# Performance work log

Hardware: AMD Instinct MI355X
Metric: run time of the kernel (lower is better)

The kernel has to match this reference:

```python
import jax, jax.numpy as jnp
import numpy as np

# Keras GRUCell (reset_after=True, default in TF2) step
# Keras LSTMCell step (gate order i, f, c, o)
# Keras RNN masking semantics: at masked steps, states are frozen and the
# step output is the previous output (equivalent to freezing every layer's h).

def _gru_step(a, h, W, U, bi, br):
    gx = a @ W + bi          # [B, 3H] input projection
    gh = h @ U + br          # [B, 3H] recurrent projection (reset_after)
    xz, xr, xh = jnp.split(gx, 3, axis=-1)
    rz, rr, rh = jnp.split(gh, 3, axis=-1)
    z = jax.nn.sigmoid(xz + rz)
    r = jax.nn.sigmoid(xr + rr)
    hh = jnp.tanh(xh + r * rh)
    return z * h + (1.0 - z) * hh


def _lstm_step(a, h, c, W, U, b):
    g = a @ W + h @ U + b    # [B, 4H]
    gi, gf, gc, go = jnp.split(g, 4, axis=-1)
    i = jax.nn.sigmoid(gi)
    f = jax.nn.sigmoid(gf)
    cn = f * c + i * jnp.tanh(gc)
    hn = jax.nn.sigmoid(go) * jnp.tanh(cn)
    return hn, cn


def run_gru_stack(x, mask, layers):
    # x: [B,T,D], mask: [B,T] bool; layers: list of (W,U,bi,br)
    B = x.shape[0]
    H = layers[0][1].shape[0]
    xT = jnp.swapaxes(x, 0, 1)      # [T,B,D]
    mT = jnp.swapaxes(mask, 0, 1)   # [T,B]

    def step(hs, inp):
        xt, mt = inp
        a = xt
        new = []
        for (W, U, bi, br), h in zip(layers, hs):
            hn = _gru_step(a, h, W, U, bi, br)
            hn = jnp.where(mt[:, None], hn, h)  # freeze state under mask
            new.append(hn)
            a = hn
        return tuple(new), a

    h0 = tuple(jnp.zeros((B, H), x.dtype) for _ in layers)
    _, ys = jax.lax.scan(step, h0, (xT, mT))
    return jnp.swapaxes(ys, 0, 1)   # [B,T,H]


def run_lstm_stack(x, mask, layers):
    # layers: list of (W,U,b)
    B = x.shape[0]
    H = layers[0][1].shape[0]
    xT = jnp.swapaxes(x, 0, 1)
    mT = jnp.swapaxes(mask, 0, 1)

    def step(state, inp):
        xt, mt = inp
        a = xt
        new = []
        for (W, U, b), (h, c) in zip(layers, state):
            hn, cn = _lstm_step(a, h, c, W, U, b)
            hn = jnp.where(mt[:, None], hn, h)
            cn = jnp.where(mt[:, None], cn, c)
            new.append((hn, cn))
            a = hn
        return tuple(new), a

    s0 = tuple((jnp.zeros((B, H), x.dtype), jnp.zeros((B, H), x.dtype)) for _ in layers)
    _, ys = jax.lax.scan(step, s0, (xT, mT))
    return jnp.swapaxes(ys, 0, 1)


def _forward(x, lengths, g_W0, g_U0, g_bi0, g_br0, g_W1, g_U1, g_bi1, g_br1,
             l_W0, l_U0, l_b0, l_W1, l_U1, l_b1, out_W, out_b):
    T = x.shape[1]
    mask = jnp.arange(T)[None, :] < lengths[:, None]          # [B,T]
    o1 = run_gru_stack(x, mask, [(g_W0, g_U0, g_bi0, g_br0),
                                 (g_W1, g_U1, g_bi1, g_br1)])  # [B,T,H]
    o2 = run_lstm_stack(x, mask, [(l_W0, l_U0, l_b0),
                                  (l_W1, l_U1, l_b1)])          # [B,T,H]
    c = jnp.concatenate([o1, o2], axis=-1)                      # [B,T,2H]
    return c @ out_W + out_b                                    # [B,T,1]


def setup_inputs() -> dict:
    key = jax.random.key(0)
    ks = jax.random.split(key, 16)
    B, T, D, H = 64, 512, 96, 256
    glorot = lambda k, shp: (jax.random.normal(k, shp, dtype=jnp.float32)
                             / np.sqrt(shp[0]).astype(np.float32))
    inp = {
        "x": jax.random.normal(ks[0], (B, T, D), dtype=jnp.float32),
        "lengths": jax.random.randint(ks[1], (B,), 1, T + 1),
        # GRU stack (reset_after: separate input/recurrent biases)
        "g_W0": glorot(ks[2], (D, 3 * H)),
        "g_U0": glorot(ks[3], (H, 3 * H)),
        "g_bi0": jnp.zeros((3 * H,), jnp.float32),
        "g_br0": jnp.zeros((3 * H,), jnp.float32),
        "g_W1": glorot(ks[4], (H, 3 * H)),
        "g_U1": glorot(ks[5], (H, 3 * H)),
        "g_bi1": jnp.zeros((3 * H,), jnp.float32),
        "g_br1": jnp.zeros((3 * H,), jnp.float32),
        # LSTM stack
        "l_W0": glorot(ks[6], (D, 4 * H)),
        "l_U0": glorot(ks[7], (H, 4 * H)),
        "l_b0": jnp.zeros((4 * H,), jnp.float32),
        "l_W1": glorot(ks[8], (H, 4 * H)),
        "l_U1": glorot(ks[9], (H, 4 * H)),
        "l_b1": jnp.zeros((4 * H,), jnp.float32),
        # Dense head on concat [.., 2H] -> 1
        "out_W": glorot(ks[10], (2 * H, 1)),
        "out_b": jnp.zeros((1,), jnp.float32),
    }
    return inp


def reference(x, lengths, g_W0, g_U0, g_bi0, g_br0, g_W1, g_U1, g_bi1, g_br1,
              l_W0, l_U0, l_b0, l_W1, l_U1, l_b1, out_W, out_b):
    return _forward(x, lengths, g_W0, g_U0, g_bi0, g_br0, g_W1, g_U1, g_bi1,
                    g_br1, l_W0, l_U0, l_b0, l_W1, l_U1, l_b1, out_W, out_b)
```

## Files before the change

kernel.cpp:

```cpp
#include <hip/hip_runtime.h>
#include <hip/hip_fp16.h>

constexpr int Tt = 512, Dd = 96, Hh = 256;
constexpr int NS0 = 16;
constexpr int NSP = 8;
typedef unsigned long long u64;

constexpr size_t OFF_P0  = (size_t)4 << 20;
constexpr size_t OFF_P1  = (size_t)12 << 20;
constexpr size_t OFF_FLG = (size_t)20 << 20;
constexpr size_t OFF_W16 = ((size_t)20 << 20) + ((size_t)64 << 10);
constexpr size_t oGW0 = 0;
constexpr size_t oGU0 = oGW0 + (size_t)48 * 768;
constexpr size_t oGW1 = oGU0 + (size_t)128 * 768;
constexpr size_t oGU1 = oGW1 + (size_t)128 * 768;
constexpr size_t oLW0 = oGU1 + (size_t)128 * 768;
constexpr size_t oLU0 = oLW0 + (size_t)48 * 1024;
constexpr size_t oLW1 = oLU0 + (size_t)128 * 1024;
constexpr size_t oLU1 = oLW1 + (size_t)128 * 1024;

constexpr int SMEM_BYTES = 2048 + 65536 + 64;

__device__ __forceinline__ float sigf(float v) { return 1.0f / (1.0f + __expf(-v)); }
__device__ __forceinline__ u64 agld(const u64* p) {
    return __hip_atomic_load(p, __ATOMIC_RELAXED, __HIP_MEMORY_SCOPE_AGENT);
}
__device__ __forceinline__ int agldi(const int* p) {
    return __hip_atomic_load(p, __ATOMIC_ACQUIRE, __HIP_MEMORY_SCOPE_AGENT);
}
__device__ __forceinline__ void agst(u64* p, u64 v) {
    __hip_atomic_store(p, v, __ATOMIC_RELAXED, __HIP_MEMORY_SCOPE_AGENT);
}

__device__ __forceinline__ float dot2f(unsigned w, unsigned a, float acc) {
#if __has_builtin(__builtin_amdgcn_fdot2)
    typedef _Float16 h2v __attribute__((ext_vector_type(2)));
    h2v wh, ah;
    __builtin_memcpy(&wh, &w, 4);
    __builtin_memcpy(&ah, &a, 4);
    return __builtin_amdgcn_fdot2(wh, ah, acc, false);
#else
    const float2 wf = __half22float2(*(const __half2*)&w);
    const float2 af = __half22float2(*(const __half2*)&a);
    acc = fmaf(wf.x, af.x, acc);
    return fmaf(wf.y, af.y, acc);
#endif
}

__device__ __forceinline__ int hidx(int k, int r) {
    return (k >> 1) * 8 + r * 2 + (k & 1);
}

template<int G>
__device__ __forceinline__ void load4h(uint4* wv, const uint4* __restrict__ M4,
                                       int ldm, int kpb) {
    const int base = (kpb >> 2) * ldm;
    #pragma unroll
    for (int g = 0; g < G; ++g)
        wv[g] = M4[base + g * 256];
}
template<int G>
__device__ __forceinline__ void fma4h(const uint4* wv, const uint4* __restrict__ A4,
                                      int kpb, float4* acc) {
    const uint4 a0 = A4[kpb + 0];
    const uint4 a1 = A4[kpb + 1];
    const uint4 a2 = A4[kpb + 2];
    const uint4 a3 = A4[kpb + 3];
    #pragma unroll
    for (int g = 0; g < G; ++g) {
        const uint4 w = wv[g];
        acc[g].x = dot2f(w.x, a0.x, acc[g].x);
        acc[g].y = dot2f(w.x, a0.y, acc[g].y);
        acc[g].z = dot2f(w.x, a0.z, acc[g].z);
        acc[g].w = dot2f(w.x, a0.w, acc[g].w);
        acc[g].x = dot2f(w.y, a1.x, acc[g].x);
        acc[g].y = dot2f(w.y, a1.y, acc[g].y);
        acc[g].z = dot2f(w.y, a1.z, acc[g].z);
        acc[g].w = dot2f(w.y, a1.w, acc[g].w);
        acc[g].x = dot2f(w.z, a2.x, acc[g].x);
        acc[g].y = dot2f(w.z, a2.y, acc[g].y);
        acc[g].z = dot2f(w.z, a2.z, acc[g].z);
        acc[g].w = dot2f(w.z, a2.w, acc[g].w);
        acc[g].x = dot2f(w.w, a3.x, acc[g].x);
        acc[g].y = dot2f(w.w, a3.y, acc[g].y);
        acc[g].z = dot2f(w.w, a3.z, acc[g].z);
        acc[g].w = dot2f(w.w, a3.w, acc[g].w);
    }
}
template<int G>
__device__ __forceinline__ void gemmP(const uint4* __restrict__ M4, int ldm,
                                      const uint4* __restrict__ A4,
                                      int kp0, int kp1, float4* acc) {
    const int n4 = (kp1 - kp0) >> 2;
    uint4 wv0[G], wv1[G];
    if (n4 <= 0) return;
    load4h<G>(wv0, M4, ldm, kp0);
    int c2 = 0;
    for (; c2 + 2 <= n4; c2 += 2) {
        load4h<G>(wv1, M4, ldm, kp0 + (c2 + 1) * 4);
        fma4h<G>(wv0, A4, kp0 + c2 * 4, acc);
        if (c2 + 2 < n4) load4h<G>(wv0, M4, ldm, kp0 + (c2 + 2) * 4);
        fma4h<G>(wv1, A4, kp0 + (c2 + 1) * 4, acc);
    }
    if (c2 < n4) fma4h<G>(wv0, A4, kp0 + c2 * 4, acc);
}

__global__ void cvt_pair(const float* __restrict__ src, unsigned* __restrict__ dst,
                         int n, int ld) {
    const int i = blockIdx.x * 256 + threadIdx.x;
    if (i >= n) return;
    const int kp = i / ld, col = i - kp * ld;
    const __half2 h = __floats2half2_rn(src[(2 * kp) * ld + col],
                                        src[(2 * kp + 1) * ld + col]);
    dst[((size_t)((kp >> 2) * ld + col) << 2) + (kp & 3)] = *(const unsigned*)&h;
}

__global__ void __launch_bounds__(1024, 4)
rnn_persist(const float* __restrict__ x, const int* __restrict__ lengths,
            const float* __restrict__ gbi0, const float* __restrict__ gbr0,
            const float* __restrict__ gbi1, const float* __restrict__ gbr1,
            const float* __restrict__ lb0, const float* __restrict__ lb1,
            const float* __restrict__ outW, const float* __restrict__ outb,
            float* __restrict__ out, char* __restrict__ wsb)
{
    extern __shared__ __align__(16) char smem[];
    unsigned* sAh = (unsigned*)smem;
    float* sG   = (float*)(smem + 2048);
    float* sRed = (float*)(smem + 2048 + 65536);
    __half* sAhh = (__half*)sAh;
    const uint4* A4 = (const uint4*)sAh;

    const int tid = threadIdx.x;
    const int c   = tid & 255;
    const int grp = tid >> 8;
    const int bx  = blockIdx.x;
    const int role  = bx & 3;
    const int chain = (bx >> 2) & 1;
    const int rg    = bx >> 3;
    const int rowbase = rg * 4;

    const int GA  = chain ? 4 : 3;
    const int GAH = GA * Hh;

    u64* h0ring = (u64*)wsb + (size_t)(chain * 16 + rg) * (NS0 * 1024);
    u64* p0ring = (u64*)(wsb + OFF_P0) + (size_t)(chain * 16 + rg) * (NSP * 4096);
    u64* p1ring = (u64*)(wsb + OFF_P1) + (size_t)(chain * 16 + rg) * (NSP * 4096);
    int* flags = (int*)(wsb + OFF_FLG);
    int* flg_r0 = flags + ((chain * 16 + rg) * 4 + 1) * 32;
    int* flg_p1 = flags + ((chain * 16 + rg) * 4 + 2) * 32;
    int* flg_r1 = flags + ((chain * 16 + rg) * 4 + 3) * 32;

    const unsigned* W16 = (const unsigned*)(wsb + OFF_W16);
    size_t woff;
    if (chain == 0) woff = (role == 0) ? oGW0 : (role == 1) ? oGU0 : (role == 2) ? oGW1 : oGU1;
    else            woff = (role == 0) ? oLW0 : (role == 1) ? oLU0 : (role == 2) ? oLW1 : oLU1;
    const uint4* M4 = (const uint4*)(W16 + woff) + c;

    const int KR  = (role == 0) ? Dd : Hh;
    const int KP2 = KR >> 3;
    const int kp0 = grp * KP2, kp1 = kp0 + KP2;

    const int NP  = 4 * GAH;
    const int npt = NP >> 10;
    float biasv[4];
    int sgidx[4];
    if (role == 0 || role == 2) {
        const float* bsrc = (chain == 0) ? (role == 0 ? gbi0 : gbi1)
                                         : (role == 0 ? lb0 : lb1);
        #pragma unroll
        for (int i = 0; i < 4; ++i) {
            if (i < npt) {
                const int e = tid + i * 1024;
                const int r = e / GAH, rem = e - r * GAH;
                biasv[i] = bsrc[rem];
                sgidx[i] = r * 1024 + rem;
            } else { biasv[i] = 0; sgidx[i] = 0; }
        }
    }
    const int rA = grp;
    const int lenA = lengths[rowbase + rA];
    float brz = 0, brr = 0, brh = 0, ow = 0;
    if (chain == 0 && (role == 1 || role == 3)) {
        const float* br = (role == 1) ? gbr0 : gbr1;
        brz = br[c]; brr = br[Hh + c]; brh = br[2 * Hh + c];
    }
    if (role == 3) ow = outW[chain * Hh + c];
    const float outb0 = outb[0];
    float creg = 0.0f;
    float hprev = 0.0f;

    for (int i = tid; i < 512; i += 1024) sAh[i] = 0;
    __syncthreads();

    for (int t = 0; t < Tt; ++t) {
        const u64* pslot = nullptr;
        u64 pr[4] = {0, 0, 0, 0};
        if (role == 1 || role == 3) {
            pslot = ((role == 1) ? p0ring : p1ring)
                    + (size_t)(t & (NSP - 1)) * 4096 + rA * GAH + c;
            #pragma unroll
            for (int g = 0; g < 4; ++g)
                if (g < GA) pr[g] = agld(pslot + g * 256);
        }

        if (role == 0) {
            if (t >= NSP) {
                if (tid == 0)
                    while (agldi(flg_r0) < t - NSP + 1) __builtin_amdgcn_s_sleep(1);
                __syncthreads();
            }
            if (tid < 4 * Dd) {
                const int r = tid / Dd, k = tid - r * Dd;
                const float v = x[((size_t)(rowbase + r) * Tt + t) * Dd + k];
                sAhh[hidx(k, r)] = __float2half(v);
            }
            __syncthreads();
        } else if (role == 2) {
            const u64* p0 = h0ring + (size_t)(t & (NS0 - 1)) * 1024 + rA * 256 + c;
            const unsigned want = (unsigned)(t + 1);
            u64 v0;
            do { v0 = agld(p0); } while ((unsigned)v0 != want);
            sAhh[hidx(c, rA)] = __float2half(__uint_as_float((unsigned)(v0 >> 32)));
            __syncthreads();
            if (tid == 0)
                __hip_atomic_exchange(flg_p1, t + 1, __ATOMIC_RELEASE,
                                      __HIP_MEMORY_SCOPE_AGENT);
        }

        {
            const int b = grp * 4096;
            if (chain == 0) {
                float4 acc[3] = {{0,0,0,0},{0,0,0,0},{0,0,0,0}};
                gemmP<3>(M4, GAH, A4, kp0, kp1, acc);
                #pragma unroll
                for (int g = 0; g < 3; ++g) {
                    sG[b + 0 + g * 256 + c]    = acc[g].x;
                    sG[b + 1024 + g * 256 + c] = acc[g].y;
                    sG[b + 2048 + g * 256 + c] = acc[g].z;
                    sG[b + 3072 + g * 256 + c] = acc[g].w;
                }
            } else {
                float4 acc[4] = {{0,0,0,0},{0,0,0,0},{0,0,0,0},{0,0,0,0}};
                gemmP<4>(M4, GAH, A4, kp0, kp1, acc);
                #pragma unroll
                for (int g = 0; g < 4; ++g) {
                    sG[b + 0 + g * 256 + c]    = acc[g].x;
                    sG[b + 1024 + g * 256 + c] = acc[g].y;
                    sG[b + 2048 + g * 256 + c] = acc[g].z;
                    sG[b + 3072 + g * 256 + c] = acc[g].w;
                }
            }
        }
        __syncthreads();

        #define SUM4(i) ((sG[(i)] + sG[8192 + (i)]) + (sG[4096 + (i)] + sG[12288 + (i)]))

        if (role == 0 || role == 2) {
            if (role == 2 && t >= NSP) {
                if (tid == 0)
                    while (agldi(flg_r1) < t - NSP + 1) __builtin_amdgcn_s_sleep(1);
                __syncthreads();
            }
            u64* ring = (role == 0) ? p0ring : p1ring;
            u64* slot = ring + (size_t)(t & (NSP - 1)) * 4096;
            for (int i = 0; i < npt; ++i) {
                const float v = SUM4(sgidx[i]) + biasv[i];
                agst(slot + tid + i * 1024,
                     ((u64)__float_as_uint(v) << 32) | (unsigned)(t + 1));
            }
        } else {
            const unsigned want = (unsigned)(t + 1);
            float P_[4] = {0, 0, 0, 0};
            #pragma unroll
            for (int g = 0; g < 4; ++g) {
                if (g < GA) {
                    u64 v = pr[g];
                    while ((unsigned)v != want) v = agld(pslot + g * 256);
                    P_[g] = __uint_as_float((unsigned)(v >> 32));
                }
            }
            if (role == 1 && t >= NS0) {
                if (tid == 0)
                    while (agldi(flg_p1) < t - NS0 + 1) __builtin_amdgcn_s_sleep(1);
                __syncthreads();
            }
            const int r = rA;
            const float hold = hprev;
            float hn;
            if (chain == 0) {
                const float Qz = SUM4(r * 1024 + c);
                const float Qr = SUM4(r * 1024 + 256 + c);
                const float Qh = SUM4(r * 1024 + 512 + c);
                const float z  = sigf(P_[0] + Qz + brz);
                const float rr = sigf(P_[1] + Qr + brr);
                const float hh = tanhf(P_[2] + rr * (Qh + brh));
                hn = z * hold + (1.0f - z) * hh;
                if (t >= lenA) hn = hold;
            } else {
                const float gi = P_[0] + SUM4(r * 1024 + c);
                const float gf = P_[1] + SUM4(r * 1024 + 256 + c);
                const float gc = P_[2] + SUM4(r * 1024 + 512 + c);
                const float go = P_[3] + SUM4(r * 1024 + 768 + c);
                float cn = sigf(gf) * creg + sigf(gi) * tanhf(gc);
                hn = sigf(go) * tanhf(cn);
                if (t >= lenA) { hn = hold; cn = creg; }
                creg = cn;
            }
            hprev = hn;
            sAhh[hidx(c, r)] = __float2half(hn);
            if (role == 1) {
                agst(h0ring + (size_t)(t & (NS0 - 1)) * 1024 + r * 256 + c,
                     ((u64)__float_as_uint(hn) << 32) | (unsigned)(t + 1));
            } else {
                float vh = hn * ow;
                for (int o = 32; o > 0; o >>= 1)
                    vh += __shfl_down(vh, o);
                if ((tid & 63) == 0) sRed[tid >> 6] = vh;
                __syncthreads();
                if (tid < 4) {
                    const float s = sRed[tid * 4] + sRed[tid * 4 + 1]
                                  + sRed[tid * 4 + 2] + sRed[tid * 4 + 3];
                    atomicAdd(&out[(size_t)(rowbase + tid) * Tt + t],
                              s + (chain ? outb0 : 0.0f));
                }
            }
        }
        #undef SUM4
        __syncthreads();
        if (tid == 0 && (role == 1 || role == 3)) {
            __hip_atomic_exchange((role == 1) ? flg_r0 : flg_r1, t + 1,
                                  __ATOMIC_RELEASE, __HIP_MEMORY_SCOPE_AGENT);
        }
    }
}

extern "C" void kernel_launch(void* const* d_in, const int* in_sizes, int n_in,
                              void* d_out, int out_size, void* d_ws, size_t ws_size,
                              hipStream_t stream) {
    const float* x       = (const float*)d_in[0];
    const int*   lengths = (const int*)d_in[1];
    const float* gW0  = (const float*)d_in[2];
    const float* gU0  = (const float*)d_in[3];
    const float* gbi0 = (const float*)d_in[4];
    const float* gbr0 = (const float*)d_in[5];
    const float* gW1  = (const float*)d_in[6];
    const float* gU1  = (const float*)d_in[7];
    const float* gbi1 = (const float*)d_in[8];
    const float* gbr1 = (const float*)d_in[9];
    const float* lW0  = (const float*)d_in[10];
    const float* lU0  = (const float*)d_in[11];
    const float* lb0  = (const float*)d_in[12];
    const float* lW1  = (const float*)d_in[13];
    const float* lU1  = (const float*)d_in[14];
    const float* lb1  = (const float*)d_in[15];
    const float* outW = (const float*)d_in[16];
    const float* outb = (const float*)d_in[17];
    float* out = (float*)d_out;
    char* wsb  = (char*)d_ws;

    hipMemsetAsync(d_ws, 0, OFF_FLG + (16 << 10), stream);
    hipMemsetAsync(d_out, 0, (size_t)out_size * sizeof(float), stream);

    unsigned* W16 = (unsigned*)(wsb + OFF_W16);
    struct { const float* s; size_t o; int K; int ld; } cv[8] = {
        {gW0, oGW0, 96, 768}, {gU0, oGU0, 256, 768},
        {gW1, oGW1, 256, 768}, {gU1, oGU1, 256, 768},
        {lW0, oLW0, 96, 1024}, {lU0, oLU0, 256, 1024},
        {lW1, oLW1, 256, 1024}, {lU1, oLU1, 256, 1024},
    };
    for (int i = 0; i < 8; ++i) {
        const int n = (cv[i].K / 2) * cv[i].ld;
        cvt_pair<<<(n + 255) / 256, 256, 0, stream>>>(cv[i].s, W16 + cv[i].o, n, cv[i].ld);
    }

    (void)hipFuncSetAttribute((const void*)rnn_persist,
                              hipFuncAttributeMaxDynamicSharedMemorySize, SMEM_BYTES);
    rnn_persist<<<dim3(128), dim3(1024), SMEM_BYTES, stream>>>(
        x, lengths, gbi0, gbr0, gbi1, gbr1, lb0, lb1, outW, outb, out, wsb);
}
```

Baseline: 5.431 ms.

## Pin leading weight chunks in LDS and reduce gate partials with shared atomics

Each block copies its first NRES k-chunks of fp16 weights into LDS once, before the time loop. It then streams only the remaining chunks from a compacted global copy written by the conversion kernel. The four per-group partial-sum buffers are replaced by one LDS buffer accumulated with shared-memory atomicAdd and re-zeroed by its consumers. The early prefetch of the projection ring is replaced by a masked polling loop placed after the GEMM. The aim is to cut repeated per-timestep global/L2 weight traffic, at the cost of LDS atomic contention, a much larger LDS footprint and the loss of the overlapped ring prefetch.

```diff
diff --git a/kernel.cpp b/kernel.cpp
--- a/kernel.cpp
+++ b/kernel.cpp
@@ -10,6 +10,7 @@
 constexpr size_t OFF_P1  = (size_t)12 << 20;
 constexpr size_t OFF_FLG = (size_t)20 << 20;
 constexpr size_t OFF_W16 = ((size_t)20 << 20) + ((size_t)64 << 10);
+constexpr size_t OFF_WST = (size_t)24 << 20;
 constexpr size_t oGW0 = 0;
 constexpr size_t oGU0 = oGW0 + (size_t)48 * 768;
 constexpr size_t oGW1 = oGU0 + (size_t)128 * 768;
@@ -19,7 +20,8 @@
 constexpr size_t oLW1 = oLU0 + (size_t)128 * 1024;
 constexpr size_t oLU1 = oLW1 + (size_t)128 * 1024;
 
-constexpr int SMEM_BYTES = 2048 + 65536 + 64;
+constexpr int SMEM_HDR   = 2048 + 16384 + 64;
+constexpr int SMEM_BYTES = SMEM_HDR + 11 * 768 * 16;
 
 __device__ __forceinline__ float sigf(float v) { return 1.0f / (1.0f + __expf(-v)); }
 __device__ __forceinline__ u64 agld(const u64* p) {
@@ -105,14 +107,18 @@
     if (c2 < n4) fma4h<G>(wv0, A4, kp0 + c2 * 4, acc);
 }
 
-__global__ void cvt_pair(const float* __restrict__ src, unsigned* __restrict__ dst,
-                         int n, int ld) {
+__global__ void cvt_pair(const float* __restrict__ src, unsigned* __restrict__ dstF,
+                         unsigned* __restrict__ dstS, int n, int ld, int nres) {
     const int i = blockIdx.x * 256 + threadIdx.x;
     if (i >= n) return;
     const int kp = i / ld, col = i - kp * ld;
     const __half2 h = __floats2half2_rn(src[(2 * kp) * ld + col],
                                         src[(2 * kp + 1) * ld + col]);
-    dst[((size_t)((kp >> 2) * ld + col) << 2) + (kp & 3)] = *(const unsigned*)&h;
+    const unsigned u = *(const unsigned*)&h;
+    const int kpc = kp >> 2;
+    dstF[((size_t)(kpc * ld + col) << 2) + (kp & 3)] = u;
+    if (kpc >= nres)
+        dstS[((size_t)((kpc - nres) * ld + col) << 2) + (kp & 3)] = u;
 }
 
 __global__ void __launch_bounds__(1024, 4)
@@ -126,7 +132,8 @@
     extern __shared__ __align__(16) char smem[];
     unsigned* sAh = (unsigned*)smem;
     float* sG   = (float*)(smem + 2048);
-    float* sRed = (float*)(smem + 2048 + 65536);
+    float* sRed = (float*)(smem + 2048 + 16384);
+    uint4* Wlds = (uint4*)(smem + SMEM_HDR);
     __half* sAhh = (__half*)sAh;
     const uint4* A4 = (const uint4*)sAh;
 
@@ -151,14 +158,19 @@
     int* flg_r1 = flags + ((chain * 16 + rg) * 4 + 3) * 32;
 
     const unsigned* W16 = (const unsigned*)(wsb + OFF_W16);
+    const unsigned* WST = (const unsigned*)(wsb + OFF_WST);
     size_t woff;
     if (chain == 0) woff = (role == 0) ? oGW0 : (role == 1) ? oGU0 : (role == 2) ? oGW1 : oGU1;
     else            woff = (role == 0) ? oLW0 : (role == 1) ? oLU0 : (role == 2) ? oLW1 : oLU1;
-    const uint4* M4 = (const uint4*)(W16 + woff) + c;
-
-    const int KR  = (role == 0) ? Dd : Hh;
-    const int KP2 = KR >> 3;
-    const int kp0 = grp * KP2, kp1 = kp0 + KP2;
+    const uint4* Mfull = (const uint4*)(W16 + woff);
+    const uint4* M4S   = (const uint4*)(WST + woff) + c;
+
+    const int KR   = (role == 0) ? Dd : Hh;
+    const int NKPC = KR >> 3;
+    const int NRES = min(chain == 0 ? 11 : 8, NKPC);
+    const int NSTR = NKPC - NRES;
+    const int dlo = (grp * NSTR) >> 2, dhi = ((grp + 1) * NSTR) >> 2;
+    const int rlo = (grp * NRES) >> 2, rhi = ((grp + 1) * NRES) >> 2;
 
     const int NP  = 4 * GAH;
     const int npt = NP >> 10;
@@ -190,19 +202,11 @@
     float hprev = 0.0f;
 
     for (int i = tid; i < 512; i += 1024) sAh[i] = 0;
+    for (int i = tid; i < 4096; i += 1024) sG[i] = 0.0f;
+    for (int i = tid; i < NRES * GAH; i += 1024) Wlds[i] = Mfull[i];
     __syncthreads();
 
     for (int t = 0; t < Tt; ++t) {
-        const u64* pslot = nullptr;
-        u64 pr[4] = {0, 0, 0, 0};
-        if (role == 1 || role == 3) {
-            pslot = ((role == 1) ? p0ring : p1ring)
-                    + (size_t)(t & (NSP - 1)) * 4096 + rA * GAH + c;
-            #pragma unroll
-            for (int g = 0; g < 4; ++g)
-                if (g < GA) pr[g] = agld(pslot + g * 256);
-        }
-
         if (role == 0) {
             if (t >= NSP) {
                 if (tid == 0)
@@ -227,33 +231,42 @@
                                       __HIP_MEMORY_SCOPE_AGENT);
         }
 
-        {
-            const int b = grp * 4096;
-            if (chain == 0) {
-                float4 acc[3] = {{0,0,0,0},{0,0,0,0},{0,0,0,0}};
-                gemmP<3>(M4, GAH, A4, kp0, kp1, acc);
+        if (chain == 0) {
+            float4 acc[3] = {{0,0,0,0},{0,0,0,0},{0,0,0,0}};
+            gemmP<3>(M4S, GAH, A4 + NRES * 4, dlo * 4, dhi * 4, acc);
+            for (int cb = rlo; cb < rhi; ++cb) {
+                uint4 w[3];
                 #pragma unroll
-                for (int g = 0; g < 3; ++g) {
-                    sG[b + 0 + g * 256 + c]    = acc[g].x;
-                    sG[b + 1024 + g * 256 + c] = acc[g].y;
-                    sG[b + 2048 + g * 256 + c] = acc[g].z;
-                    sG[b + 3072 + g * 256 + c] = acc[g].w;
-                }
-            } else {
-                float4 acc[4] = {{0,0,0,0},{0,0,0,0},{0,0,0,0},{0,0,0,0}};
-                gemmP<4>(M4, GAH, A4, kp0, kp1, acc);
+                for (int g = 0; g < 3; ++g)
+                    w[g] = Wlds[(size_t)cb * GAH + g * 256 + c];
+                fma4h<3>(w, A4, cb * 4, acc);
+            }
+            #pragma unroll
+            for (int g = 0; g < 3; ++g) {
+                atomicAdd(&sG[0    + g * 256 + c], acc[g].x);
+                atomicAdd(&sG[1024 + g * 256 + c], acc[g].y);
+                atomicAdd(&sG[2048 + g * 256 + c], acc[g].z);
+                atomicAdd(&sG[3072 + g * 256 + c], acc[g].w);
+            }
+        } else {
+            float4 acc[4] = {{0,0,0,0},{0,0,0,0},{0,0,0,0},{0,0,0,0}};
+            gemmP<4>(M4S, GAH, A4 + NRES * 4, dlo * 4, dhi * 4, acc);
+            for (int cb = rlo; cb < rhi; ++cb) {
+                uint4 w[4];
                 #pragma unroll
-                for (int g = 0; g < 4; ++g) {
-                    sG[b + 0 + g * 256 + c]    = acc[g].x;
-                    sG[b + 1024 + g * 256 + c] = acc[g].y;
-                    sG[b + 2048 + g * 256 + c] = acc[g].z;
-                    sG[b + 3072 + g * 256 + c] = acc[g].w;
-                }
+                for (int g = 0; g < 4; ++g)
+                    w[g] = Wlds[(size_t)cb * GAH + g * 256 + c];
+                fma4h<4>(w, A4, cb * 4, acc);
+            }
+            #pragma unroll
+            for (int g = 0; g < 4; ++g) {
+                atomicAdd(&sG[0    + g * 256 + c], acc[g].x);
+                atomicAdd(&sG[1024 + g * 256 + c], acc[g].y);
+                atomicAdd(&sG[2048 + g * 256 + c], acc[g].z);
+                atomicAdd(&sG[3072 + g * 256 + c], acc[g].w);
             }
         }
         __syncthreads();
-
-        #define SUM4(i) ((sG[(i)] + sG[8192 + (i)]) + (sG[4096 + (i)] + sG[12288 + (i)]))
 
         if (role == 0 || role == 2) {
             if (role == 2 && t >= NSP) {
@@ -264,19 +277,28 @@
             u64* ring = (role == 0) ? p0ring : p1ring;
             u64* slot = ring + (size_t)(t & (NSP - 1)) * 4096;
             for (int i = 0; i < npt; ++i) {
-                const float v = SUM4(sgidx[i]) + biasv[i];
+                const float v = sG[sgidx[i]] + biasv[i];
+                sG[sgidx[i]] = 0.0f;
                 agst(slot + tid + i * 1024,
                      ((u64)__float_as_uint(v) << 32) | (unsigned)(t + 1));
             }
         } else {
+            const u64* slot = ((role == 1) ? p0ring : p1ring)
+                              + (size_t)(t & (NSP - 1)) * 4096 + rA * GAH + c;
             const unsigned want = (unsigned)(t + 1);
             float P_[4] = {0, 0, 0, 0};
-            #pragma unroll
-            for (int g = 0; g < 4; ++g) {
-                if (g < GA) {
-                    u64 v = pr[g];
-                    while ((unsigned)v != want) v = agld(pslot + g * 256);
-                    P_[g] = __uint_as_float((unsigned)(v >> 32));
+            unsigned dm = 0;
+            const unsigned full = (1u << GA) - 1u;
+            while (dm != full) {
+                #pragma unroll
+                for (int g = 0; g < 4; ++g) {
+                    if (g < GA && !(dm & (1u << g))) {
+                        const u64 v = agld(slot + g * 256);
+                        if ((unsigned)v == want) {
+                            P_[g] = __uint_as_float((unsigned)(v >> 32));
+                            dm |= 1u << g;
+                        }
+                    }
                 }
             }
             if (role == 1 && t >= NS0) {
@@ -285,22 +307,27 @@
                 __syncthreads();
             }
             const int r = rA;
+            const int qb = r * 1024 + c;
             const float hold = hprev;
             float hn;
             if (chain == 0) {
-                const float Qz = SUM4(r * 1024 + c);
-                const float Qr = SUM4(r * 1024 + 256 + c);
-                const float Qh = SUM4(r * 1024 + 512 + c);
+                const float Qz = sG[qb];       sG[qb] = 0.0f;
+                const float Qr = sG[qb + 256]; sG[qb + 256] = 0.0f;
+                const float Qh = sG[qb + 512]; sG[qb + 512] = 0.0f;
                 const float z  = sigf(P_[0] + Qz + brz);
                 const float rr = sigf(P_[1] + Qr + brr);
                 const float hh = tanhf(P_[2] + rr * (Qh + brh));
                 hn = z * hold + (1.0f - z) * hh;
                 if (t >= lenA) hn = hold;
             } else {
-                const float gi = P_[0] + SUM4(r * 1024 + c);
-                const float gf = P_[1] + SUM4(r * 1024 + 256 + c);
-                const float gc = P_[2] + SUM4(r * 1024 + 512 + c);
-                const float go = P_[3] + SUM4(r * 1024 + 768 + c);
+                const float Q0 = sG[qb];       sG[qb] = 0.0f;
+                const float Q1 = sG[qb + 256]; sG[qb + 256] = 0.0f;
+                const float Q2 = sG[qb + 512]; sG[qb + 512] = 0.0f;
+                const float Q3 = sG[qb + 768]; sG[qb + 768] = 0.0f;
+                const float gi = P_[0] + Q0;
+                const float gf = P_[1] + Q1;
+                const float gc = P_[2] + Q2;
+                const float go = P_[3] + Q3;
                 float cn = sigf(gf) * creg + sigf(gi) * tanhf(gc);
                 hn = sigf(go) * tanhf(cn);
                 if (t >= lenA) { hn = hold; cn = creg; }
@@ -325,7 +352,6 @@
                 }
             }
         }
-        #undef SUM4
         __syncthreads();
         if (tid == 0 && (role == 1 || role == 3)) {
             __hip_atomic_exchange((role == 1) ? flg_r0 : flg_r1, t + 1,
@@ -362,6 +388,7 @@
     hipMemsetAsync(d_out, 0, (size_t)out_size * sizeof(float), stream);
 
     unsigned* W16 = (unsigned*)(wsb + OFF_W16);
+    unsigned* WST = (unsigned*)(wsb + OFF_WST);
     struct { const float* s; size_t o; int K; int ld; } cv[8] = {
         {gW0, oGW0, 96, 768}, {gU0, oGU0, 256, 768},
         {gW1, oGW1, 256, 768}, {gU1, oGU1, 256, 768},
@@ -370,7 +397,9 @@
     };
     for (int i = 0; i < 8; ++i) {
         const int n = (cv[i].K / 2) * cv[i].ld;
-        cvt_pair<<<(n + 255) / 256, 256, 0, stream>>>(cv[i].s, W16 + cv[i].o, n, cv[i].ld);
+        const int nres = (cv[i].ld == 768) ? 11 : 8;
+        cvt_pair<<<(n + 255) / 256, 256, 0, stream>>>(
+            cv[i].s, W16 + cv[i].o, WST + cv[i].o, n, cv[i].ld, nres);
     }
 
     (void)hipFuncSetAttribute((const void*)rnn_persist,
```

New measurement: 14.73 ms. +171.3%, slower.
